# Kernel optimization log

Hardware: AMD Instinct MI355X
Metric: run time of the kernel (lower is better)

## Reference

```python
import jax, jax.numpy as jnp
import numpy as np

GROUP = 64   # quantization group size (nunchaku W4A4 default)
QMAX = 7.0   # symmetric int4 positive range


def setup_inputs() -> dict:
    key = jax.random.key(0)
    ks = jax.random.split(key, 6)
    T, K, N, R = 256, 3072, 3072, 32
    x = jax.random.normal(ks[0], (T, K), dtype=jnp.float32)
    # int4 weight codes stored as 0..15 (dequant subtracts zero-point 8)
    qweight = jax.random.randint(ks[1], (N, K), 0, 16, dtype=jnp.int32)
    # per-(out_channel, input_group) weight scales, small positive
    wscales = jax.random.uniform(ks[2], (N, K // GROUP), dtype=jnp.float32) * 0.02 + 1e-3
    lora_down = jax.random.normal(ks[3], (R, K), dtype=jnp.float32) / np.sqrt(K)
    lora_up = jax.random.normal(ks[4], (N, R), dtype=jnp.float32) / np.sqrt(R)
    bias = jax.random.normal(ks[5], (N,), dtype=jnp.float32) * 0.01
    return {"x": x, "qweight": qweight, "wscales": wscales,
            "lora_down": lora_down, "lora_up": lora_up, "bias": bias}


def _quantize_act(x):
    # per-token, per-group symmetric int4 fake-quant (quantize -> dequantize)
    T, K = x.shape
    xg = x.reshape(T, K // GROUP, GROUP)
    scale = jnp.maximum(jnp.max(jnp.abs(xg), axis=-1, keepdims=True) / QMAX, 1e-8)
    q = jnp.clip(jnp.round(xg / scale), -8.0, QMAX)
    return (q * scale).reshape(T, K)


def reference(x, qweight, wscales, lora_down, lora_up, bias):
    # Dequantize int4 weights: (code - 8) * per-group scale  -> [N, K]
    N, K = qweight.shape
    w = (qweight.astype(jnp.float32) - 8.0).reshape(N, K // GROUP, GROUP)
    w = (w * wscales[:, :, None]).reshape(N, K)
    # W4A4 main path: int4-quantized activations x dequantized int4 weights
    x_dq = _quantize_act(x)
    main = x_dq @ w.T                               # [T, N]
    # fused low-rank (SVDQuant LoRA) branch on full-precision activations
    lora = (x @ lora_down.T) @ lora_up.T            # [T, R] @ [R, N]
    return main + lora + bias
```

## Files before the change

### kernel.cpp

```cpp
#include <hip/hip_runtime.h>
#include <stdint.h>

#define T_DIM 256
#define K_DIM 3072
#define N_DIM 3072
#define R_DIM 32
#define KG    48
#define NSPLIT 4

#define PQ_BLOCKS 2304
#define QA_BLOCKS 3072
#define LM_BLOCKS 96

typedef __bf16 bf16x8 __attribute__((ext_vector_type(8)));
typedef float  f32x4  __attribute__((ext_vector_type(4)));
typedef unsigned short u16x8 __attribute__((ext_vector_type(8)));
typedef int    v4i    __attribute__((ext_vector_type(4)));

__device__ __forceinline__ unsigned short f2bf(float f) {
    unsigned u = __builtin_bit_cast(unsigned, f);
    unsigned rounding = 0x7FFFu + ((u >> 16) & 1u);
    return (unsigned short)((u + rounding) >> 16);
}

__device__ __forceinline__ bf16x8 cvt8(const float* p) {
    float4 lo = ((const float4*)p)[0], hi = ((const float4*)p)[1];
    u16x8 u;
    u[0] = f2bf(lo.x); u[1] = f2bf(lo.y); u[2] = f2bf(lo.z); u[3] = f2bf(lo.w);
    u[4] = f2bf(hi.x); u[5] = f2bf(hi.y); u[6] = f2bf(hi.z); u[7] = f2bf(hi.w);
    return __builtin_bit_cast(bf16x8, u);
}

__device__ __forceinline__ unsigned pack4m8(int4 c) {
    return (unsigned)((c.x - 8) & 255) | ((unsigned)((c.y - 8) & 255) << 8)
         | ((unsigned)((c.z - 8) & 255) << 16) | ((unsigned)((c.w - 8) & 255) << 24);
}

__global__ __launch_bounds__(256) void prep(
        const int*   __restrict__ qweight,
        const float* __restrict__ wscales,
        const float* __restrict__ x,
        const float* __restrict__ lora_down,
        signed char* __restrict__ Qb,
        float*       __restrict__ Sw,
        signed char* __restrict__ Aq,
        float*       __restrict__ Sa,
        float*       __restrict__ Lm) {
    int blk = blockIdx.x;
    if (blk < PQ_BLOCKS) {
        size_t i = (size_t)blk * 256 + threadIdx.x;
        const int4* p = (const int4*)(qweight + i * 16);
        uint4 w;
        w.x = pack4m8(p[0]); w.y = pack4m8(p[1]);
        w.z = pack4m8(p[2]); w.w = pack4m8(p[3]);
        int n  = (int)(i / 192);
        int kw = (int)(i % 192);
        int kt = kw >> 2;
        int ko = (kw & 3) * 16;
        *(uint4*)(Qb + ((size_t)kt * N_DIM + n) * 64 + ko) = w;
        if ((kw & 3) == 0) Sw[(size_t)kt * N_DIM + n] = wscales[(size_t)n * KG + kt];
    } else if (blk < PQ_BLOCKS + QA_BLOCKS) {
        int widx = (blk - PQ_BLOCKS) * 4 + (threadIdx.x >> 6);
        int lane = threadIdx.x & 63;
        int t = widx / KG, g = widx % KG;
        float v = x[(size_t)t * K_DIM + g * 64 + lane];
        float a = fabsf(v);
        #pragma unroll
        for (int off = 32; off; off >>= 1) a = fmaxf(a, __shfl_xor(a, off));
        float scale = fmaxf(a / 7.0f, 1e-8f);
        float q = rintf(v / scale);
        q = fminf(fmaxf(q, -8.f), 7.f);
        Aq[((size_t)g * 256 + t) * 64 + lane] = (signed char)(int)q;
        if (lane == 0) Sa[(size_t)g * 256 + t] = scale;
    } else {
        int kb = blk - PQ_BLOCKS - QA_BLOCKS;
        int lane = threadIdx.x & 63, wv = threadIdx.x >> 6;
        int mrow = lane & 15, quad = lane >> 4;
        int k0 = kb * 32 + quad * 8;
        bf16x8 a[4], b[2];
        #pragma unroll
        for (int mt = 0; mt < 4; ++mt)
            a[mt] = cvt8(x + (size_t)(wv * 64 + mt * 16 + mrow) * K_DIM + k0);
        #pragma unroll
        for (int nt = 0; nt < 2; ++nt)
            b[nt] = cvt8(lora_down + (size_t)(nt * 16 + mrow) * K_DIM + k0);
        f32x4 acc[4][2];
        f32x4 zero = {0.f, 0.f, 0.f, 0.f};
        #pragma unroll
        for (int i = 0; i < 4; ++i) { acc[i][0] = zero; acc[i][1] = zero; }
        #pragma unroll
        for (int mt = 0; mt < 4; ++mt)
            #pragma unroll
            for (int nt = 0; nt < 2; ++nt)
                acc[mt][nt] = __builtin_amdgcn_mfma_f32_16x16x32_bf16(
                    a[mt], b[nt], acc[mt][nt], 0, 0, 0);
        #pragma unroll
        for (int mt = 0; mt < 4; ++mt)
            #pragma unroll
            for (int nt = 0; nt < 2; ++nt)
                #pragma unroll
                for (int r = 0; r < 4; ++r)
                    atomicAdd(&Lm[(size_t)(wv * 64 + mt * 16 + quad * 4 + r) * R_DIM
                                  + nt * 16 + mrow], acc[mt][nt][r]);
    }
}

__global__ __launch_bounds__(256) void gemm_main(
        const signed char* __restrict__ Aq,
        const signed char* __restrict__ Qb,
        const float*       __restrict__ Sa,
        const float*       __restrict__ Sw,
        const float*       __restrict__ Lm,
        const float*       __restrict__ lora_up,
        float*             __restrict__ P) {
    int nblk  = blockIdx.x;
    int mblk  = blockIdx.y;
    int split = blockIdx.z;
    int c0 = split * (KG / NSPLIT);
    int tid = threadIdx.x;
    int lane = tid & 63, wv = tid >> 6;
    int mrow = lane & 15, quad = lane >> 4;
    const int nbase = nblk * 64;
    const int mbase = mblk * 128 + wv * 32;

    f32x4 acc[2][4];
    f32x4 fzero = {0.f, 0.f, 0.f, 0.f};
    #pragma unroll
    for (int i = 0; i < 2; ++i)
        #pragma unroll
        for (int j = 0; j < 4; ++j) acc[i][j] = fzero;

    #pragma unroll 3
    for (int kk = c0; kk < c0 + KG / NSPLIT; ++kk) {
        const signed char* aB = Aq + (size_t)kk * (256 * 64);
        const signed char* bB = Qb + (size_t)kk * ((size_t)N_DIM * 64);
        v4i a[2], b[4];
        #pragma unroll
        for (int mt = 0; mt < 2; ++mt)
            a[mt] = *(const v4i*)(aB + (size_t)(mbase + mt * 16 + mrow) * 64 + quad * 16);
        #pragma unroll
        for (int nt = 0; nt < 4; ++nt)
            b[nt] = *(const v4i*)(bB + (size_t)(nbase + nt * 16 + mrow) * 64 + quad * 16);
        float4 sa[2];
        #pragma unroll
        for (int mt = 0; mt < 2; ++mt)
            sa[mt] = *(const float4*)(Sa + (size_t)kk * 256 + mbase + mt * 16 + quad * 4);
        float sw[4];
        #pragma unroll
        for (int nt = 0; nt < 4; ++nt)
            sw[nt] = Sw[(size_t)kk * N_DIM + nbase + nt * 16 + mrow];
        #pragma unroll
        for (int mt = 0; mt < 2; ++mt)
            #pragma unroll
            for (int nt = 0; nt < 4; ++nt) {
                v4i z = {0, 0, 0, 0};
                v4i d = __builtin_amdgcn_mfma_i32_16x16x64_i8(a[mt], b[nt], z, 0, 0, 0);
                acc[mt][nt][0] += (float)d[0] * (sa[mt].x * sw[nt]);
                acc[mt][nt][1] += (float)d[1] * (sa[mt].y * sw[nt]);
                acc[mt][nt][2] += (float)d[2] * (sa[mt].z * sw[nt]);
                acc[mt][nt][3] += (float)d[3] * (sa[mt].w * sw[nt]);
            }
    }

    if (split == NSPLIT - 1) {
        bf16x8 at[2], bt[4];
        #pragma unroll
        for (int mt = 0; mt < 2; ++mt)
            at[mt] = cvt8(Lm + (size_t)(mbase + mt * 16 + mrow) * R_DIM + quad * 8);
        #pragma unroll
        for (int nt = 0; nt < 4; ++nt)
            bt[nt] = cvt8(lora_up + (size_t)(nbase + nt * 16 + mrow) * R_DIM + quad * 8);
        #pragma unroll
        for (int mt = 0; mt < 2; ++mt)
            #pragma unroll
            for (int nt = 0; nt < 4; ++nt)
                acc[mt][nt] = __builtin_amdgcn_mfma_f32_16x16x32_bf16(
                    at[mt], bt[nt], acc[mt][nt], 0, 0, 0);
    }

    float* Pp = P + (size_t)split * (T_DIM * N_DIM);
    #pragma unroll
    for (int nt = 0; nt < 4; ++nt) {
        int n = nbase + nt * 16 + mrow;
        #pragma unroll
        for (int mt = 0; mt < 2; ++mt) {
            int row0 = mblk * 128 + wv * 32 + mt * 16 + quad * 4;
            #pragma unroll
            for (int r = 0; r < 4; ++r)
                Pp[(size_t)(row0 + r) * N_DIM + n] = acc[mt][nt][r];
        }
    }
}

__global__ __launch_bounds__(256) void reduce_out(
        const float4* __restrict__ P, const float* __restrict__ bias,
        float4* __restrict__ out) {
    int i = blockIdx.x * 256 + threadIdx.x;
    const int STRIDE = T_DIM * N_DIM / 4;
    float4 bv = *(const float4*)&bias[(i * 4) % N_DIM];
    float4 o = bv;
    #pragma unroll
    for (int s = 0; s < NSPLIT; ++s) {
        float4 v = P[i + s * STRIDE];
        o.x += v.x; o.y += v.y; o.z += v.z; o.w += v.w;
    }
    out[i] = o;
}

extern "C" void kernel_launch(void* const* d_in, const int* in_sizes, int n_in,
                              void* d_out, int out_size, void* d_ws, size_t ws_size,
                              hipStream_t stream) {
    const float* x         = (const float*)d_in[0];
    const int*   qweight   = (const int*)d_in[1];
    const float* wscales   = (const float*)d_in[2];
    const float* lora_down = (const float*)d_in[3];
    const float* lora_up   = (const float*)d_in[4];
    const float* bias      = (const float*)d_in[5];

    char* wsp = (char*)d_ws;
    signed char* Aq = (signed char*)wsp;  wsp += (size_t)KG * 256 * 64;
    signed char* Qb = (signed char*)wsp;  wsp += (size_t)KG * N_DIM * 64;
    float* Sa = (float*)wsp;              wsp += (size_t)KG * 256 * 4;
    float* Sw = (float*)wsp;              wsp += (size_t)KG * N_DIM * 4;
    float* Lm = (float*)wsp;              wsp += (size_t)T_DIM * R_DIM * 4;
    float* P  = (float*)wsp;

    hipMemsetAsync(Lm, 0, (size_t)T_DIM * R_DIM * sizeof(float), stream);
    prep<<<PQ_BLOCKS + QA_BLOCKS + LM_BLOCKS, 256, 0, stream>>>(
        qweight, wscales, x, lora_down, Qb, Sw, Aq, Sa, Lm);
    gemm_main<<<dim3(48, 2, NSPLIT), 256, 0, stream>>>(
        Aq, Qb, Sa, Sw, Lm, lora_up, P);
    reduce_out<<<(T_DIM * N_DIM / 4) / 256, 256, 0, stream>>>(
        (const float4*)P, bias, (float4*)d_out);
}
```

Before: 117.2 us.

## Fuse int4 weight packing into GEMM and cover all rows per block

Removes the separate weight-repacking pass from the prep kernel. The GEMM now reads the int32 weight codes and the weight scales directly and packs them to int8 in registers. Each block covers all 256 token rows, so every weight element is read only once, and the K split goes from 4 to 6 to keep enough blocks in flight. The trade-off is strided int32 global loads in the GEMM inner loop, more accumulator registers, a larger partial-sum buffer to reduce, and only 288 blocks.

```diff
diff --git a/kernel.cpp b/kernel.cpp
--- a/kernel.cpp
+++ b/kernel.cpp
@@ -6,9 +6,8 @@
 #define N_DIM 3072
 #define R_DIM 32
 #define KG    48
-#define NSPLIT 4
-
-#define PQ_BLOCKS 2304
+#define NSPLIT 6
+
 #define QA_BLOCKS 3072
 #define LM_BLOCKS 96
 
@@ -37,30 +36,14 @@
 }
 
 __global__ __launch_bounds__(256) void prep(
-        const int*   __restrict__ qweight,
-        const float* __restrict__ wscales,
         const float* __restrict__ x,
         const float* __restrict__ lora_down,
-        signed char* __restrict__ Qb,
-        float*       __restrict__ Sw,
         signed char* __restrict__ Aq,
         float*       __restrict__ Sa,
         float*       __restrict__ Lm) {
     int blk = blockIdx.x;
-    if (blk < PQ_BLOCKS) {
-        size_t i = (size_t)blk * 256 + threadIdx.x;
-        const int4* p = (const int4*)(qweight + i * 16);
-        uint4 w;
-        w.x = pack4m8(p[0]); w.y = pack4m8(p[1]);
-        w.z = pack4m8(p[2]); w.w = pack4m8(p[3]);
-        int n  = (int)(i / 192);
-        int kw = (int)(i % 192);
-        int kt = kw >> 2;
-        int ko = (kw & 3) * 16;
-        *(uint4*)(Qb + ((size_t)kt * N_DIM + n) * 64 + ko) = w;
-        if ((kw & 3) == 0) Sw[(size_t)kt * N_DIM + n] = wscales[(size_t)n * KG + kt];
-    } else if (blk < PQ_BLOCKS + QA_BLOCKS) {
-        int widx = (blk - PQ_BLOCKS) * 4 + (threadIdx.x >> 6);
+    if (blk < QA_BLOCKS) {
+        int widx = blk * 4 + (threadIdx.x >> 6);
         int lane = threadIdx.x & 63;
         int t = widx / KG, g = widx % KG;
         float v = x[(size_t)t * K_DIM + g * 64 + lane];
@@ -73,7 +56,7 @@
         Aq[((size_t)g * 256 + t) * 64 + lane] = (signed char)(int)q;
         if (lane == 0) Sa[(size_t)g * 256 + t] = scale;
     } else {
-        int kb = blk - PQ_BLOCKS - QA_BLOCKS;
+        int kb = blk - QA_BLOCKS;
         int lane = threadIdx.x & 63, wv = threadIdx.x >> 6;
         int mrow = lane & 15, quad = lane >> 4;
         int k0 = kb * 32 + quad * 8;
@@ -105,52 +88,57 @@
     }
 }
 
-__global__ __launch_bounds__(256) void gemm_main(
+__global__ __launch_bounds__(256, 2) void gemm_main(
         const signed char* __restrict__ Aq,
-        const signed char* __restrict__ Qb,
+        const int*         __restrict__ qweight,
+        const float*       __restrict__ wscales,
         const float*       __restrict__ Sa,
-        const float*       __restrict__ Sw,
         const float*       __restrict__ Lm,
         const float*       __restrict__ lora_up,
         float*             __restrict__ P) {
     int nblk  = blockIdx.x;
-    int mblk  = blockIdx.y;
-    int split = blockIdx.z;
+    int split = blockIdx.y;
     int c0 = split * (KG / NSPLIT);
     int tid = threadIdx.x;
     int lane = tid & 63, wv = tid >> 6;
     int mrow = lane & 15, quad = lane >> 4;
     const int nbase = nblk * 64;
-    const int mbase = mblk * 128 + wv * 32;
-
-    f32x4 acc[2][4];
+
+    f32x4 acc[4][4];
     f32x4 fzero = {0.f, 0.f, 0.f, 0.f};
     #pragma unroll
-    for (int i = 0; i < 2; ++i)
+    for (int i = 0; i < 4; ++i)
         #pragma unroll
         for (int j = 0; j < 4; ++j) acc[i][j] = fzero;
 
-    #pragma unroll 3
+    #pragma unroll 2
     for (int kk = c0; kk < c0 + KG / NSPLIT; ++kk) {
-        const signed char* aB = Aq + (size_t)kk * (256 * 64);
-        const signed char* bB = Qb + (size_t)kk * ((size_t)N_DIM * 64);
-        v4i a[2], b[4];
-        #pragma unroll
-        for (int mt = 0; mt < 2; ++mt)
-            a[mt] = *(const v4i*)(aB + (size_t)(mbase + mt * 16 + mrow) * 64 + quad * 16);
+        v4i b[4];
+        #pragma unroll
+        for (int nt = 0; nt < 4; ++nt) {
+            const int4* qp = (const int4*)(qweight
+                + (size_t)(nbase + nt * 16 + mrow) * K_DIM + kk * 64 + quad * 16);
+            int4 q0 = qp[0], q1 = qp[1], q2 = qp[2], q3 = qp[3];
+            uint4 w;
+            w.x = pack4m8(q0); w.y = pack4m8(q1);
+            w.z = pack4m8(q2); w.w = pack4m8(q3);
+            b[nt] = __builtin_bit_cast(v4i, w);
+        }
+        v4i a[4];
+        #pragma unroll
+        for (int mt = 0; mt < 4; ++mt)
+            a[mt] = *(const v4i*)(Aq
+                + ((size_t)kk * 256 + (wv * 64 + mt * 16 + mrow)) * 64 + quad * 16);
+        float4 sa[4];
+        #pragma unroll
+        for (int mt = 0; mt < 4; ++mt)
+            sa[mt] = *(const float4*)(Sa + (size_t)kk * 256 + wv * 64 + mt * 16 + quad * 4);
+        float sw[4];
         #pragma unroll
         for (int nt = 0; nt < 4; ++nt)
-            b[nt] = *(const v4i*)(bB + (size_t)(nbase + nt * 16 + mrow) * 64 + quad * 16);
-        float4 sa[2];
-        #pragma unroll
-        for (int mt = 0; mt < 2; ++mt)
-            sa[mt] = *(const float4*)(Sa + (size_t)kk * 256 + mbase + mt * 16 + quad * 4);
-        float sw[4];
-        #pragma unroll
-        for (int nt = 0; nt < 4; ++nt)
-            sw[nt] = Sw[(size_t)kk * N_DIM + nbase + nt * 16 + mrow];
-        #pragma unroll
-        for (int mt = 0; mt < 2; ++mt)
+            sw[nt] = wscales[(size_t)(nbase + nt * 16 + mrow) * KG + kk];
+        #pragma unroll
+        for (int mt = 0; mt < 4; ++mt)
             #pragma unroll
             for (int nt = 0; nt < 4; ++nt) {
                 v4i z = {0, 0, 0, 0};
@@ -163,15 +151,15 @@
     }
 
     if (split == NSPLIT - 1) {
-        bf16x8 at[2], bt[4];
-        #pragma unroll
-        for (int mt = 0; mt < 2; ++mt)
-            at[mt] = cvt8(Lm + (size_t)(mbase + mt * 16 + mrow) * R_DIM + quad * 8);
+        bf16x8 at[4], bt[4];
+        #pragma unroll
+        for (int mt = 0; mt < 4; ++mt)
+            at[mt] = cvt8(Lm + (size_t)(wv * 64 + mt * 16 + mrow) * R_DIM + quad * 8);
         #pragma unroll
         for (int nt = 0; nt < 4; ++nt)
             bt[nt] = cvt8(lora_up + (size_t)(nbase + nt * 16 + mrow) * R_DIM + quad * 8);
         #pragma unroll
-        for (int mt = 0; mt < 2; ++mt)
+        for (int mt = 0; mt < 4; ++mt)
             #pragma unroll
             for (int nt = 0; nt < 4; ++nt)
                 acc[mt][nt] = __builtin_amdgcn_mfma_f32_16x16x32_bf16(
@@ -183,8 +171,8 @@
     for (int nt = 0; nt < 4; ++nt) {
         int n = nbase + nt * 16 + mrow;
         #pragma unroll
-        for (int mt = 0; mt < 2; ++mt) {
-            int row0 = mblk * 128 + wv * 32 + mt * 16 + quad * 4;
+        for (int mt = 0; mt < 4; ++mt) {
+            int row0 = wv * 64 + mt * 16 + quad * 4;
             #pragma unroll
             for (int r = 0; r < 4; ++r)
                 Pp[(size_t)(row0 + r) * N_DIM + n] = acc[mt][nt][r];
@@ -219,17 +207,14 @@
 
     char* wsp = (char*)d_ws;
     signed char* Aq = (signed char*)wsp;  wsp += (size_t)KG * 256 * 64;
-    signed char* Qb = (signed char*)wsp;  wsp += (size_t)KG * N_DIM * 64;
     float* Sa = (float*)wsp;              wsp += (size_t)KG * 256 * 4;
-    float* Sw = (float*)wsp;              wsp += (size_t)KG * N_DIM * 4;
     float* Lm = (float*)wsp;              wsp += (size_t)T_DIM * R_DIM * 4;
     float* P  = (float*)wsp;
 
     hipMemsetAsync(Lm, 0, (size_t)T_DIM * R_DIM * sizeof(float), stream);
-    prep<<<PQ_BLOCKS + QA_BLOCKS + LM_BLOCKS, 256, 0, stream>>>(
-        qweight, wscales, x, lora_down, Qb, Sw, Aq, Sa, Lm);
-    gemm_main<<<dim3(48, 2, NSPLIT), 256, 0, stream>>>(
-        Aq, Qb, Sa, Sw, Lm, lora_up, P);
+    prep<<<QA_BLOCKS + LM_BLOCKS, 256, 0, stream>>>(x, lora_down, Aq, Sa, Lm);
+    gemm_main<<<dim3(48, NSPLIT), 256, 0, stream>>>(
+        Aq, qweight, wscales, Sa, Lm, lora_up, P);
     reduce_out<<<(T_DIM * N_DIM / 4) / 256, 256, 0, stream>>>(
         (const float4*)P, bias, (float4*)d_out);
 }
```

Result: slower. 154.9 us (+32.2%).

## Move split-K reduction into LDS within GEMM block and drop reduce kernel

Applied to the files above, without the earlier changes.

The split-K partitioning moves from separate grid blocks writing fp32 partials to global memory into the four waves of one block. Each wave now computes a 64x64 tile over a quarter of K, and the waves reduce through shared memory, with bias added in the epilogue. This removes the reduce_out kernel and the 12 MB partial buffer round trip. Weight scales are also read directly from wscales rather than through a transposed Sw copy. The trade-off is fewer blocks (192 instead of 384), about 66 KB of LDS per block, and a strided wscales access pattern.

```diff
diff --git a/kernel.cpp b/kernel.cpp
--- a/kernel.cpp
+++ b/kernel.cpp
@@ -6,7 +6,6 @@
 #define N_DIM 3072
 #define R_DIM 32
 #define KG    48
-#define NSPLIT 4
 
 #define PQ_BLOCKS 2304
 #define QA_BLOCKS 3072
@@ -38,11 +37,9 @@
 
 __global__ __launch_bounds__(256) void prep(
         const int*   __restrict__ qweight,
-        const float* __restrict__ wscales,
         const float* __restrict__ x,
         const float* __restrict__ lora_down,
         signed char* __restrict__ Qb,
-        float*       __restrict__ Sw,
         signed char* __restrict__ Aq,
         float*       __restrict__ Sa,
         float*       __restrict__ Lm) {
@@ -58,7 +55,6 @@
         int kt = kw >> 2;
         int ko = (kw & 3) * 16;
         *(uint4*)(Qb + ((size_t)kt * N_DIM + n) * 64 + ko) = w;
-        if ((kw & 3) == 0) Sw[(size_t)kt * N_DIM + n] = wscales[(size_t)n * KG + kt];
     } else if (blk < PQ_BLOCKS + QA_BLOCKS) {
         int widx = (blk - PQ_BLOCKS) * 4 + (threadIdx.x >> 6);
         int lane = threadIdx.x & 63;
@@ -108,49 +104,48 @@
 __global__ __launch_bounds__(256) void gemm_main(
         const signed char* __restrict__ Aq,
         const signed char* __restrict__ Qb,
+        const float*       __restrict__ wscales,
         const float*       __restrict__ Sa,
-        const float*       __restrict__ Sw,
         const float*       __restrict__ Lm,
         const float*       __restrict__ lora_up,
-        float*             __restrict__ P) {
-    int nblk  = blockIdx.x;
-    int mblk  = blockIdx.y;
-    int split = blockIdx.z;
-    int c0 = split * (KG / NSPLIT);
+        const float*       __restrict__ bias,
+        float*             __restrict__ out) {
+    __shared__ float Ls[4][64 * 65];
+    int nblk = blockIdx.x, mblk = blockIdx.y;
     int tid = threadIdx.x;
     int lane = tid & 63, wv = tid >> 6;
     int mrow = lane & 15, quad = lane >> 4;
-    const int nbase = nblk * 64;
-    const int mbase = mblk * 128 + wv * 32;
-
-    f32x4 acc[2][4];
+    const int nbase = nblk * 64, mbase = mblk * 64;
+    const int c0 = wv * (KG / 4);
+
+    f32x4 acc[4][4];
     f32x4 fzero = {0.f, 0.f, 0.f, 0.f};
     #pragma unroll
-    for (int i = 0; i < 2; ++i)
+    for (int i = 0; i < 4; ++i)
         #pragma unroll
         for (int j = 0; j < 4; ++j) acc[i][j] = fzero;
 
     #pragma unroll 3
-    for (int kk = c0; kk < c0 + KG / NSPLIT; ++kk) {
-        const signed char* aB = Aq + (size_t)kk * (256 * 64);
-        const signed char* bB = Qb + (size_t)kk * ((size_t)N_DIM * 64);
-        v4i a[2], b[4];
-        #pragma unroll
-        for (int mt = 0; mt < 2; ++mt)
-            a[mt] = *(const v4i*)(aB + (size_t)(mbase + mt * 16 + mrow) * 64 + quad * 16);
-        #pragma unroll
-        for (int nt = 0; nt < 4; ++nt)
-            b[nt] = *(const v4i*)(bB + (size_t)(nbase + nt * 16 + mrow) * 64 + quad * 16);
-        float4 sa[2];
-        #pragma unroll
-        for (int mt = 0; mt < 2; ++mt)
+    for (int kk = c0; kk < c0 + KG / 4; ++kk) {
+        v4i a[4], b[4];
+        #pragma unroll
+        for (int nt = 0; nt < 4; ++nt)
+            b[nt] = *(const v4i*)(Qb
+                + ((size_t)kk * N_DIM + nbase + nt * 16 + mrow) * 64 + quad * 16);
+        #pragma unroll
+        for (int mt = 0; mt < 4; ++mt)
+            a[mt] = *(const v4i*)(Aq
+                + ((size_t)kk * 256 + mbase + mt * 16 + mrow) * 64 + quad * 16);
+        float4 sa[4];
+        #pragma unroll
+        for (int mt = 0; mt < 4; ++mt)
             sa[mt] = *(const float4*)(Sa + (size_t)kk * 256 + mbase + mt * 16 + quad * 4);
         float sw[4];
         #pragma unroll
         for (int nt = 0; nt < 4; ++nt)
-            sw[nt] = Sw[(size_t)kk * N_DIM + nbase + nt * 16 + mrow];
-        #pragma unroll
-        for (int mt = 0; mt < 2; ++mt)
+            sw[nt] = wscales[(size_t)(nbase + nt * 16 + mrow) * KG + kk];
+        #pragma unroll
+        for (int mt = 0; mt < 4; ++mt)
             #pragma unroll
             for (int nt = 0; nt < 4; ++nt) {
                 v4i z = {0, 0, 0, 0};
@@ -162,49 +157,46 @@
             }
     }
 
-    if (split == NSPLIT - 1) {
-        bf16x8 at[2], bt[4];
-        #pragma unroll
-        for (int mt = 0; mt < 2; ++mt)
+    if (wv == 3) {
+        bf16x8 at[4], bt[4];
+        #pragma unroll
+        for (int mt = 0; mt < 4; ++mt)
             at[mt] = cvt8(Lm + (size_t)(mbase + mt * 16 + mrow) * R_DIM + quad * 8);
         #pragma unroll
         for (int nt = 0; nt < 4; ++nt)
             bt[nt] = cvt8(lora_up + (size_t)(nbase + nt * 16 + mrow) * R_DIM + quad * 8);
         #pragma unroll
-        for (int mt = 0; mt < 2; ++mt)
+        for (int mt = 0; mt < 4; ++mt)
             #pragma unroll
             for (int nt = 0; nt < 4; ++nt)
                 acc[mt][nt] = __builtin_amdgcn_mfma_f32_16x16x32_bf16(
                     at[mt], bt[nt], acc[mt][nt], 0, 0, 0);
     }
 
-    float* Pp = P + (size_t)split * (T_DIM * N_DIM);
     #pragma unroll
-    for (int nt = 0; nt < 4; ++nt) {
-        int n = nbase + nt * 16 + mrow;
-        #pragma unroll
-        for (int mt = 0; mt < 2; ++mt) {
-            int row0 = mblk * 128 + wv * 32 + mt * 16 + quad * 4;
+    for (int mt = 0; mt < 4; ++mt)
+        #pragma unroll
+        for (int nt = 0; nt < 4; ++nt)
             #pragma unroll
             for (int r = 0; r < 4; ++r)
-                Pp[(size_t)(row0 + r) * N_DIM + n] = acc[mt][nt][r];
+                Ls[wv][(mt * 16 + quad * 4 + r) * 65 + nt * 16 + mrow] = acc[mt][nt][r];
+    __syncthreads();
+
+    int r0 = tid >> 2, cs = (tid & 3) * 16;
+    float* orow = out + (size_t)(mbase + r0) * N_DIM + nbase + cs;
+    #pragma unroll
+    for (int j = 0; j < 4; ++j) {
+        float4 o = *(const float4*)&bias[nbase + cs + j * 4];
+        #pragma unroll
+        for (int s = 0; s < 4; ++s) {
+            int base = r0 * 65 + cs + j * 4;
+            o.x += Ls[s][base + 0];
+            o.y += Ls[s][base + 1];
+            o.z += Ls[s][base + 2];
+            o.w += Ls[s][base + 3];
         }
-    }
-}
-
-__global__ __launch_bounds__(256) void reduce_out(
-        const float4* __restrict__ P, const float* __restrict__ bias,
-        float4* __restrict__ out) {
-    int i = blockIdx.x * 256 + threadIdx.x;
-    const int STRIDE = T_DIM * N_DIM / 4;
-    float4 bv = *(const float4*)&bias[(i * 4) % N_DIM];
-    float4 o = bv;
-    #pragma unroll
-    for (int s = 0; s < NSPLIT; ++s) {
-        float4 v = P[i + s * STRIDE];
-        o.x += v.x; o.y += v.y; o.z += v.z; o.w += v.w;
-    }
-    out[i] = o;
+        *(float4*)(orow + j * 4) = o;
+    }
 }
 
 extern "C" void kernel_launch(void* const* d_in, const int* in_sizes, int n_in,
@@ -216,20 +208,17 @@
     const float* lora_down = (const float*)d_in[3];
     const float* lora_up   = (const float*)d_in[4];
     const float* bias      = (const float*)d_in[5];
+    float* out = (float*)d_out;
 
     char* wsp = (char*)d_ws;
     signed char* Aq = (signed char*)wsp;  wsp += (size_t)KG * 256 * 64;
     signed char* Qb = (signed char*)wsp;  wsp += (size_t)KG * N_DIM * 64;
     float* Sa = (float*)wsp;              wsp += (size_t)KG * 256 * 4;
-    float* Sw = (float*)wsp;              wsp += (size_t)KG * N_DIM * 4;
-    float* Lm = (float*)wsp;              wsp += (size_t)T_DIM * R_DIM * 4;
-    float* P  = (float*)wsp;
+    float* Lm = (float*)wsp;
 
     hipMemsetAsync(Lm, 0, (size_t)T_DIM * R_DIM * sizeof(float), stream);
     prep<<<PQ_BLOCKS + QA_BLOCKS + LM_BLOCKS, 256, 0, stream>>>(
-        qweight, wscales, x, lora_down, Qb, Sw, Aq, Sa, Lm);
-    gemm_main<<<dim3(48, 2, NSPLIT), 256, 0, stream>>>(
-        Aq, Qb, Sa, Sw, Lm, lora_up, P);
-    reduce_out<<<(T_DIM * N_DIM / 4) / 256, 256, 0, stream>>>(
-        (const float4*)P, bias, (float4*)d_out);
-}
+        qweight, x, lora_down, Qb, Aq, Sa, Lm);
+    gemm_main<<<dim3(48, 4), 256, 0, stream>>>(
+        Aq, Qb, wscales, Sa, Lm, lora_up, bias, out);
+}
```

Measured after the change: 118.7 us. Within noise of the previous version (+1.3%).
